# Kernel tuning notes

Measured on AMD Instinct MI355X. Metric: run time of the kernel, lower is better.

Reference implementation:

```python
import jax, jax.numpy as jnp
import numpy as np

N_NODES = 20000
N_EDGES = 320000
IN_DIM = 512
NUM_CLASSES = 10
DROP_P = 0.2


def _gcn_conv(x, src, dst, W, b, n):
    # PyG GCNConv: linear transform, add self-loops, symmetric deg^-1/2 norm,
    # scatter-add into destination nodes, then bias.
    h = x @ W                                   # [N, out]
    loops = jnp.arange(n)
    s = jnp.concatenate([src, loops])           # source (j)
    d = jnp.concatenate([dst, loops])           # destination (i)
    deg = jax.ops.segment_sum(jnp.ones_like(s, dtype=h.dtype), d, num_segments=n)
    dinv = jax.lax.rsqrt(deg)                   # deg >= 1 thanks to self-loops
    norm = dinv[s] * dinv[d]                    # [E+N]
    msg = h[s] * norm[:, None]                  # gather + per-edge scale
    out = jax.ops.segment_sum(msg, d, num_segments=n)  # scatter-add
    return out + b


def _dropout(x, key, p=DROP_P):
    keep = jax.random.bernoulli(key, 1.0 - p, x.shape)
    return jnp.where(keep, x / (1.0 - p), jnp.zeros((), x.dtype))


def setup_inputs() -> dict:
    key = jax.random.key(0)
    ks = jax.random.split(key, 6)
    x = jax.random.normal(ks[0], (N_NODES, IN_DIM), dtype=jnp.float32)
    edge_index = jax.random.randint(ks[1], (2, N_EDGES), 0, N_NODES, dtype=jnp.int64)
    h1, h2 = IN_DIM // 2, IN_DIM // 4
    W1 = jax.random.normal(ks[2], (IN_DIM, h1), dtype=jnp.float32) / np.sqrt(IN_DIM)
    W2 = jax.random.normal(ks[3], (h1, h2), dtype=jnp.float32) / np.sqrt(h1)
    W3 = jax.random.normal(ks[4], (h2, NUM_CLASSES), dtype=jnp.float32) / np.sqrt(h2)
    b1 = jnp.zeros((h1,), jnp.float32)
    b2 = jnp.zeros((h2,), jnp.float32)
    b3 = jnp.zeros((NUM_CLASSES,), jnp.float32)
    return {"x": x, "edge_index": edge_index, "W1": W1, "b1": b1,
            "W2": W2, "b2": b2, "W3": W3, "b3": b3}


def reference(x, edge_index, W1, b1, W2, b2, W3, b3):
    n = x.shape[0]
    src, dst = edge_index[0], edge_index[1]
    dk1, dk2 = jax.random.split(jax.random.key(1))
    h = _gcn_conv(x, src, dst, W1, b1, n)
    h = _dropout(jax.nn.relu(h), dk1)
    h = _gcn_conv(h, src, dst, W2, b2, n)
    h = _dropout(jax.nn.relu(h), dk2)
    h = _gcn_conv(h, src, dst, W3, b3, n)
    return jax.nn.log_softmax(h, axis=1)
```

## Files before the change

kernel.cpp:

```cpp
#include <hip/hip_runtime.h>
#include <hip/hip_bf16.h>
#include <math.h>

typedef __attribute__((ext_vector_type(8))) short short8;
typedef __attribute__((ext_vector_type(8))) unsigned short ushort8;
typedef __attribute__((ext_vector_type(4))) float f32x4;

__host__ __device__ inline void threefry2x32(unsigned k0, unsigned k1,
                                             unsigned x0, unsigned x1,
                                             unsigned* out0, unsigned* out1) {
  unsigned ks0 = k0, ks1 = k1, ks2 = k0 ^ k1 ^ 0x1BD11BDAu;
  x0 += ks0; x1 += ks1;
#define TF_ROUND(r) { x0 += x1; x1 = (x1 << (r)) | (x1 >> (32 - (r))); x1 ^= x0; }
  TF_ROUND(13) TF_ROUND(15) TF_ROUND(26) TF_ROUND(6)
  x0 += ks1; x1 += ks2 + 1u;
  TF_ROUND(17) TF_ROUND(29) TF_ROUND(16) TF_ROUND(24)
  x0 += ks2; x1 += ks0 + 2u;
  TF_ROUND(13) TF_ROUND(15) TF_ROUND(26) TF_ROUND(6)
  x0 += ks0; x1 += ks1 + 3u;
  TF_ROUND(17) TF_ROUND(29) TF_ROUND(16) TF_ROUND(24)
  x0 += ks1; x1 += ks2 + 4u;
  TF_ROUND(13) TF_ROUND(15) TF_ROUND(26) TF_ROUND(6)
  x0 += ks2; x1 += ks0 + 5u;
#undef TF_ROUND
  *out0 = x0; *out1 = x1;
}

__device__ inline float jax_uniform01(unsigned key0, unsigned key1, unsigned i) {
  unsigned o0, o1;
  threefry2x32(key0, key1, 0u, i, &o0, &o1);
  unsigned bits = o0 ^ o1;
  return __uint_as_float((bits >> 9) | 0x3f800000u) - 1.0f;
}

__device__ inline unsigned short f2bf(float f) {
  unsigned u = __float_as_uint(f);
  u += 0x7fffu + ((u >> 16) & 1u);
  return (unsigned short)(u >> 16);
}

__device__ inline float bf2f(unsigned short b) {
  return __uint_as_float(((unsigned)b) << 16);
}

__global__ __launch_bounds__(256) void k_init(int* __restrict__ deg, int n,
                                              const float* __restrict__ W1,
                                              unsigned short* __restrict__ W1T,
                                              const float* __restrict__ W2,
                                              unsigned short* __restrict__ W2T) {
  const int S1 = 512 * 256, S2 = 256 * 128;
  int idx = blockIdx.x * 256 + threadIdx.x;
  if (idx < n) { deg[idx] = 0; return; }
  idx -= n;
  if (idx < S1) {
    int k = idx / 256, c = idx % 256;
    W1T[(size_t)c * 512 + k] = f2bf(W1[idx]);
    return;
  }
  idx -= S1;
  if (idx < S2) {
    int k = idx / 128, c = idx % 128;
    W2T[(size_t)c * 256 + k] = f2bf(W2[idx]);
  }
}

__global__ void k_deg(const int* __restrict__ ei, int E, int* __restrict__ deg) {
  int e = blockIdx.x * blockDim.x + threadIdx.x;
  if (e >= E) return;
  atomicAdd(&deg[ei[E + e]], 1);
}

__global__ __launch_bounds__(256) void k_bsum(const int* __restrict__ deg,
                                              int* __restrict__ bsum, int n) {
  int i = blockIdx.x * 256 + threadIdx.x;
  int v = (i < n) ? deg[i] : 0;
#pragma unroll
  for (int o = 32; o; o >>= 1) v += __shfl_down(v, o);
  __shared__ int ws[4];
  if ((threadIdx.x & 63) == 0) ws[threadIdx.x >> 6] = v;
  __syncthreads();
  if (threadIdx.x == 0) bsum[blockIdx.x] = ws[0] + ws[1] + ws[2] + ws[3];
}

__global__ __launch_bounds__(256) void k_scatter2(const int* __restrict__ deg,
                                                  const int* __restrict__ bsum,
                                                  int* __restrict__ off, int* __restrict__ cur,
                                                  float* __restrict__ dinv, int n) {
  int i = blockIdx.x * 256 + threadIdx.x;
  int lane = threadIdx.x & 63, w = threadIdx.x >> 6;
  int pb = 0;
  for (int k = lane; k < blockIdx.x; k += 64) pb += bsum[k];
#pragma unroll
  for (int o = 32; o; o >>= 1) pb += __shfl_xor(pb, o);

  int d = (i < n) ? deg[i] : 0;
  int inc = d;
#pragma unroll
  for (int o = 1; o < 64; o <<= 1) {
    int u = __shfl_up(inc, o);
    if (lane >= o) inc += u;
  }
  __shared__ int wsum[4];
  if (lane == 63) wsum[w] = inc;
  __syncthreads();
  int wbase = 0;
  for (int k = 0; k < w; ++k) wbase += wsum[k];
  int excl = inc - d + wbase + pb;
  if (i < n) {
    off[i] = excl;
    cur[i] = excl;
    dinv[i] = 1.0f / sqrtf((float)(d + 1));
    if (i == n - 1) off[n] = excl + d;
  }
}

__global__ void k_fill_w(const int* __restrict__ ei, int E,
                         int* __restrict__ cur, int* __restrict__ srcs,
                         float* __restrict__ wgt, const float* __restrict__ dinv) {
  int e = blockIdx.x * blockDim.x + threadIdx.x;
  if (e >= E) return;
  int s = ei[e];
  int d = ei[E + e];
  int pos = atomicAdd(&cur[d], 1);
  srcs[pos] = s;
  wgt[pos] = dinv[s] * dinv[d];
}

template <int NF, bool AF32, bool OBF>
__global__ __launch_bounds__(256) void k_gemm_mfma(const void* __restrict__ Ap,
                                                   const unsigned short* __restrict__ BT,
                                                   void* __restrict__ Cp,
                                                   int M, int N, int K) {
  constexpr int BN = 32 * NF;
  __shared__ unsigned short As[64][40];
  __shared__ unsigned short Bs[BN][40];
  const int tid = threadIdx.x;
  const int row0 = blockIdx.y * 64;
  const int col0 = blockIdx.x * BN;
  const int w = tid >> 6, lane = tid & 63;
  const int wm = w >> 1, wn = w & 1;
  const int lr = lane & 15, lk = lane >> 4;

  f32x4 acc[2][NF];
#pragma unroll
  for (int mi = 0; mi < 2; ++mi)
#pragma unroll
    for (int ni = 0; ni < NF; ++ni) acc[mi][ni] = (f32x4)0.0f;

  const int ar = tid >> 2;
  const int aseg = (tid & 3) * 8;

  for (int k0 = 0; k0 < K; k0 += 32) {
    {
      int grow = row0 + ar;
      ushort8 av = (ushort8)0;
      if (grow < M) {
        if (AF32) {
          const float* A = (const float*)Ap;
          const float* p = &A[(size_t)grow * K + k0 + aseg];
          float4 v0 = *(const float4*)p;
          float4 v1 = *(const float4*)(p + 4);
          av[0] = f2bf(v0.x); av[1] = f2bf(v0.y); av[2] = f2bf(v0.z); av[3] = f2bf(v0.w);
          av[4] = f2bf(v1.x); av[5] = f2bf(v1.y); av[6] = f2bf(v1.z); av[7] = f2bf(v1.w);
        } else {
          const unsigned short* A = (const unsigned short*)Ap;
          av = *(const ushort8*)&A[(size_t)grow * K + k0 + aseg];
        }
      }
      *(ushort8*)&As[ar][aseg] = av;
    }
#pragma unroll
    for (int p = 0; p < BN / 64; ++p) {
      int u = tid + p * 256;
      int br = u >> 2;
      int bseg = (u & 3) * 8;
      ushort8 bv = *(const ushort8*)&BT[(size_t)(col0 + br) * K + k0 + bseg];
      *(ushort8*)&Bs[br][bseg] = bv;
    }
    __syncthreads();

    short8 a[2], b[NF];
#pragma unroll
    for (int mi = 0; mi < 2; ++mi)
      a[mi] = *(const short8*)&As[wm * 32 + mi * 16 + lr][lk * 8];
#pragma unroll
    for (int ni = 0; ni < NF; ++ni)
      b[ni] = *(const short8*)&Bs[wn * (BN / 2) + ni * 16 + lr][lk * 8];
#pragma unroll
    for (int mi = 0; mi < 2; ++mi)
#pragma unroll
      for (int ni = 0; ni < NF; ++ni)
        acc[mi][ni] = __builtin_amdgcn_mfma_f32_16x16x32_bf16(a[mi], b[ni], acc[mi][ni], 0, 0, 0);
    __syncthreads();
  }

#pragma unroll
  for (int mi = 0; mi < 2; ++mi) {
    int rbase = row0 + wm * 32 + mi * 16 + lk * 4;
#pragma unroll
    for (int j = 0; j < 4; ++j) {
      int row = rbase + j;
      if (row < M) {
#pragma unroll
        for (int ni = 0; ni < NF; ++ni) {
          int col = col0 + wn * (BN / 2) + ni * 16 + lr;
          if (OBF) {
            ((unsigned short*)Cp)[(size_t)row * N + col] = f2bf(acc[mi][ni][j]);
          } else {
            ((float*)Cp)[(size_t)row * N + col] = acc[mi][ni][j];
          }
        }
      }
    }
  }
}

__global__ __launch_bounds__(256) void k_gemm(const float* __restrict__ A,
                                              const float* __restrict__ B,
                                              float* __restrict__ C,
                                              int M, int N, int K) {
  __shared__ float As[64][17];
  __shared__ float Bs[16][64];
  const int tid = threadIdx.x;
  const int tx = tid & 15, ty = tid >> 4;
  const int row0 = blockIdx.y * 64, col0 = blockIdx.x * 64;
  const int am = tid >> 2;
  const int aq = (tid & 3) * 4;
  const int bk = tid >> 4;
  const int bg = (tid & 15) * 4;
  const bool nvec = ((N & 3) == 0);
  float acc[4][4] = {{0.f}};

  for (int k0 = 0; k0 < K; k0 += 16) {
    {
      int row = row0 + am;
      if (row < M) {
        const float4 v = *reinterpret_cast<const float4*>(&A[(size_t)row * K + k0 + aq]);
        As[am][aq + 0] = v.x; As[am][aq + 1] = v.y;
        As[am][aq + 2] = v.z; As[am][aq + 3] = v.w;
      } else {
        As[am][aq + 0] = 0.f; As[am][aq + 1] = 0.f;
        As[am][aq + 2] = 0.f; As[am][aq + 3] = 0.f;
      }
    }
    {
      int krow = k0 + bk;
      if (nvec && (col0 + bg + 4 <= N)) {
        const float4 v = *reinterpret_cast<const float4*>(&B[(size_t)krow * N + col0 + bg]);
        Bs[bk][bg + 0] = v.x; Bs[bk][bg + 1] = v.y;
        Bs[bk][bg + 2] = v.z; Bs[bk][bg + 3] = v.w;
      } else {
        for (int j = 0; j < 4; ++j) {
          int col = col0 + bg + j;
          Bs[bk][bg + j] = (col < N) ? B[(size_t)krow * N + col] : 0.f;
        }
      }
    }
    __syncthreads();
#pragma unroll
    for (int kk = 0; kk < 16; ++kk) {
      float a0 = As[ty * 4 + 0][kk];
      float a1 = As[ty * 4 + 1][kk];
      float a2 = As[ty * 4 + 2][kk];
      float a3 = As[ty * 4 + 3][kk];
      float4 bv = *reinterpret_cast<const float4*>(&Bs[kk][tx * 4]);
      acc[0][0] += a0 * bv.x; acc[0][1] += a0 * bv.y; acc[0][2] += a0 * bv.z; acc[0][3] += a0 * bv.w;
      acc[1][0] += a1 * bv.x; acc[1][1] += a1 * bv.y; acc[1][2] += a1 * bv.z; acc[1][3] += a1 * bv.w;
      acc[2][0] += a2 * bv.x; acc[2][1] += a2 * bv.y; acc[2][2] += a2 * bv.z; acc[2][3] += a2 * bv.w;
      acc[3][0] += a3 * bv.x; acc[3][1] += a3 * bv.y; acc[3][2] += a3 * bv.z; acc[3][3] += a3 * bv.w;
    }
    __syncthreads();
  }

  for (int i = 0; i < 4; ++i) {
    int row = row0 + ty * 4 + i;
    if (row >= M) continue;
    for (int j = 0; j < 4; ++j) {
      int col = col0 + tx * 4 + j;
      if (col < N) C[(size_t)row * N + col] = acc[i][j];
    }
  }
}

template <int C, bool OBF>
__global__ __launch_bounds__(256) void k_agg_bf(const unsigned short* __restrict__ h,
                                                void* __restrict__ outv,
                                                const int* __restrict__ off,
                                                const int* __restrict__ srcs,
                                                const float* __restrict__ wgt,
                                                const float* __restrict__ dinv,
                                                const float* __restrict__ bias,
                                                unsigned key0, unsigned key1, int n) {
  typedef __attribute__((ext_vector_type(C))) unsigned short ushortC;
  const int node = blockIdx.x * (blockDim.x >> 6) + (threadIdx.x >> 6);
  if (node >= n) return;
  const int lane = threadIdx.x & 63;
  const int F = 64 * C;
  const float dv = dinv[node];

  float acc[C];
  {
    ushortC r = *(const ushortC*)(h + (size_t)node * F + lane * C);
    float wv = dv * dv;
#pragma unroll
    for (int j = 0; j < C; ++j) acc[j] = bf2f(r[j]) * wv;
  }
  int e = off[node];
  const int e1 = off[node + 1];
  for (; e + 8 <= e1; e += 8) {
    int s[8];
    float wv[8];
    ushortC r[8];
#pragma unroll
    for (int q = 0; q < 8; ++q) s[q] = srcs[e + q];
#pragma unroll
    for (int q = 0; q < 8; ++q) wv[q] = wgt[e + q];
#pragma unroll
    for (int q = 0; q < 8; ++q) r[q] = *(const ushortC*)(h + (size_t)s[q] * F + lane * C);
#pragma unroll
    for (int q = 0; q < 8; ++q)
#pragma unroll
      for (int j = 0; j < C; ++j) acc[j] += bf2f(r[q][j]) * wv[q];
  }
  for (; e < e1; ++e) {
    int s = srcs[e];
    float wv = wgt[e];
    ushortC r = *(const ushortC*)(h + (size_t)s * F + lane * C);
#pragma unroll
    for (int j = 0; j < C; ++j) acc[j] += bf2f(r[j]) * wv;
  }
#pragma unroll
  for (int j = 0; j < C; ++j) {
    float v = acc[j] + bias[lane * C + j];
    v = fmaxf(v, 0.0f);
    unsigned i = (unsigned)(node * F + lane * C + j);
    float u = jax_uniform01(key0, key1, i);
    v = (u < 0.8f) ? (v * 1.25f) : 0.0f;
    acc[j] = v;
  }
  if (OBF) {
    unsigned short* op = (unsigned short*)outv + (size_t)node * F + lane * C;
#pragma unroll
    for (int j = 0; j < C; ++j) op[j] = f2bf(acc[j]);
  } else {
    float* op = (float*)outv + (size_t)node * F + lane * C;
#pragma unroll
    for (int j = 0; j < C; ++j) op[j] = acc[j];
  }
}

__global__ __launch_bounds__(256) void k_agg3_lsm_v2(const float* __restrict__ h,
                                                     float* __restrict__ out,
                                                     const int* __restrict__ off,
                                                     const int* __restrict__ srcs,
                                                     const float* __restrict__ wgt,
                                                     const float* __restrict__ dinv,
                                                     const float* __restrict__ b,
                                                     int n) {
  const int node = blockIdx.x * 4 + (threadIdx.x >> 6);
  if (node >= n) return;
  const int lane = threadIdx.x & 63;
  const bool act = (lane < 10);
  const float dv = dinv[node];

  float acc = 0.0f;
  if (act) acc = h[(size_t)node * 10 + lane] * dv * dv;
  int e = off[node];
  const int e1 = off[node + 1];
  for (; e + 4 <= e1; e += 4) {
    int s0 = srcs[e + 0], s1 = srcs[e + 1], s2 = srcs[e + 2], s3 = srcs[e + 3];
    float w0 = wgt[e + 0], w1 = wgt[e + 1], w2 = wgt[e + 2], w3 = wgt[e + 3];
    if (act) {
      acc += h[(size_t)s0 * 10 + lane] * w0 + h[(size_t)s1 * 10 + lane] * w1 +
             h[(size_t)s2 * 10 + lane] * w2 + h[(size_t)s3 * 10 + lane] * w3;
    }
  }
  for (; e < e1; ++e) {
    int s = srcs[e];
    float w = wgt[e];
    if (act) acc += h[(size_t)s * 10 + lane] * w;
  }
  float v = act ? (acc + b[lane]) : -1e30f;
  float m = v;
#pragma unroll
  for (int o = 32; o; o >>= 1) m = fmaxf(m, __shfl_xor(m, o));
  float p = act ? expf(v - m) : 0.0f;
  float ssum = p;
#pragma unroll
  for (int o = 32; o; o >>= 1) ssum += __shfl_xor(ssum, o);
  float lse = m + logf(ssum);
  if (act) out[(size_t)node * 10 + lane] = v - lse;
}

extern "C" void kernel_launch(void* const* d_in, const int* in_sizes, int n_in,
                              void* d_out, int out_size, void* d_ws, size_t ws_size,
                              hipStream_t stream) {
  const float* x  = (const float*)d_in[0];
  const int*   ei = (const int*)d_in[1];
  const float* W1 = (const float*)d_in[2];
  const float* b1 = (const float*)d_in[3];
  const float* W2 = (const float*)d_in[4];
  const float* b2 = (const float*)d_in[5];
  const float* W3 = (const float*)d_in[6];
  const float* b3 = (const float*)d_in[7];
  float* out = (float*)d_out;

  const int N = 20000;
  const int E = in_sizes[1] / 2;
  const int D1 = 256, D2 = 128;
  const int NB = (N + 255) / 256;

  char* ws = (char*)d_ws;
  auto carve = [&](size_t bytes) -> char* {
    char* p = ws;
    ws += (bytes + 255) & ~(size_t)255;
    return p;
  };
  int*   deg  = (int*)carve((size_t)N * 4);
  int*   off  = (int*)carve((size_t)(N + 1) * 4);
  int*   cur  = (int*)carve((size_t)N * 4);
  float* dinv = (float*)carve((size_t)N * 4);
  int*   bsum = (int*)carve((size_t)128 * 4);
  int*   srcs = (int*)carve((size_t)E * 4);
  float* wgt  = (float*)carve((size_t)E * 4);
  unsigned short* W1T = (unsigned short*)carve((size_t)D1 * 512 * 2);
  unsigned short* W2T = (unsigned short*)carve((size_t)D2 * D1 * 2);
  unsigned short* bufHb = (unsigned short*)carve((size_t)N * D1 * 2);
  unsigned short* bufA_bf = (unsigned short*)carve((size_t)N * D1 * 2);
  float* bufA2 = (float*)bufA_bf;
  float* bufH3 = (float*)carve((size_t)N * 10 * 4);

  unsigned dk1_0, dk1_1, dk2_0, dk2_1;
  threefry2x32(0u, 1u, 0u, 0u, &dk1_0, &dk1_1);
  threefry2x32(0u, 1u, 0u, 1u, &dk2_0, &dk2_1);

  const int INIT_ITEMS = N + 512 * 256 + 256 * 128;
  k_init<<<(INIT_ITEMS + 255) / 256, 256, 0, stream>>>(deg, N, W1, W1T, W2, W2T);
  k_deg<<<(E + 255) / 256, 256, 0, stream>>>(ei, E, deg);
  k_bsum<<<NB, 256, 0, stream>>>(deg, bsum, N);
  k_scatter2<<<NB, 256, 0, stream>>>(deg, bsum, off, cur, dinv, N);
  k_fill_w<<<(E + 255) / 256, 256, 0, stream>>>(ei, E, cur, srcs, wgt, dinv);

  k_gemm_mfma<4, true, true><<<dim3(D1 / 128, (N + 63) / 64), 256, 0, stream>>>(x, W1T, bufHb, N, D1, 512);
  k_agg_bf<4, true><<<(N + 3) / 4, 256, 0, stream>>>(bufHb, bufA_bf, off, srcs, wgt, dinv, b1, dk1_0, dk1_1, N);

  k_gemm_mfma<4, false, true><<<dim3(D2 / 128, (N + 63) / 64), 256, 0, stream>>>(bufA_bf, W2T, bufHb, N, D2, D1);
  k_agg_bf<2, false><<<(N + 3) / 4, 256, 0, stream>>>(bufHb, bufA2, off, srcs, wgt, dinv, b2, dk2_0, dk2_1, N);

  k_gemm<<<dim3(1, (N + 63) / 64), 256, 0, stream>>>(bufA2, W3, bufH3, N, 10, D2);
  k_agg3_lsm_v2<<<(N + 3) / 4, 256, 0, stream>>>(bufH3, out, off, srcs, wgt, dinv, b3, N);
}
```

Baseline: 160.2 us.

## Fuse layer-2 aggregation with layer-3 linear and retile MFMA GEMM

Layer-2 aggregation, bias, ReLU and dropout are fused with the 128x10 layer-3 matmul. Each wavefront reduces its node's 128 features against W3 with shuffle reductions and writes only the 10 outputs. This removes the fp32 intermediate buffer round trip and the separate scalar GEMM kernel. The MFMA GEMM is also retiled to 32-row blocks covering the full output width, so A is read once per row block, at the cost of less reuse per block and a grid that assumes N is divisible by 32.

```diff
diff --git a/kernel.cpp b/kernel.cpp
--- a/kernel.cpp
+++ b/kernel.cpp
@@ -4,6 +4,7 @@
 
 typedef __attribute__((ext_vector_type(8))) short short8;
 typedef __attribute__((ext_vector_type(8))) unsigned short ushort8;
+typedef __attribute__((ext_vector_type(4))) unsigned short ushort4v;
 typedef __attribute__((ext_vector_type(4))) float f32x4;
 
 __host__ __device__ inline void threefry2x32(unsigned k0, unsigned k1,
@@ -126,48 +127,46 @@
   wgt[pos] = dinv[s] * dinv[d];
 }
 
-template <int NF, bool AF32, bool OBF>
+template <int BN, bool AF32, bool OBF>
 __global__ __launch_bounds__(256) void k_gemm_mfma(const void* __restrict__ Ap,
                                                    const unsigned short* __restrict__ BT,
                                                    void* __restrict__ Cp,
                                                    int M, int N, int K) {
-  constexpr int BN = 32 * NF;
-  __shared__ unsigned short As[64][40];
+  constexpr int WCOLS = BN / 4;
+  constexpr int NFW = WCOLS / 16;
+  __shared__ unsigned short As[32][40];
   __shared__ unsigned short Bs[BN][40];
   const int tid = threadIdx.x;
-  const int row0 = blockIdx.y * 64;
+  const int row0 = blockIdx.y * 32;
   const int col0 = blockIdx.x * BN;
-  const int w = tid >> 6, lane = tid & 63;
-  const int wm = w >> 1, wn = w & 1;
+  const int wn = tid >> 6, lane = tid & 63;
   const int lr = lane & 15, lk = lane >> 4;
 
-  f32x4 acc[2][NF];
+  f32x4 acc[2][NFW];
 #pragma unroll
   for (int mi = 0; mi < 2; ++mi)
 #pragma unroll
-    for (int ni = 0; ni < NF; ++ni) acc[mi][ni] = (f32x4)0.0f;
-
-  const int ar = tid >> 2;
-  const int aseg = (tid & 3) * 8;
+    for (int ni = 0; ni < NFW; ++ni) acc[mi][ni] = (f32x4)0.0f;
+
+  const int ar = tid >> 3;
+  const int aseg = (tid & 7) * 4;
 
   for (int k0 = 0; k0 < K; k0 += 32) {
     {
       int grow = row0 + ar;
-      ushort8 av = (ushort8)0;
+      unsigned short a4[4] = {0, 0, 0, 0};
       if (grow < M) {
         if (AF32) {
           const float* A = (const float*)Ap;
-          const float* p = &A[(size_t)grow * K + k0 + aseg];
-          float4 v0 = *(const float4*)p;
-          float4 v1 = *(const float4*)(p + 4);
-          av[0] = f2bf(v0.x); av[1] = f2bf(v0.y); av[2] = f2bf(v0.z); av[3] = f2bf(v0.w);
-          av[4] = f2bf(v1.x); av[5] = f2bf(v1.y); av[6] = f2bf(v1.z); av[7] = f2bf(v1.w);
+          float4 v = *(const float4*)&A[(size_t)grow * K + k0 + aseg];
+          a4[0] = f2bf(v.x); a4[1] = f2bf(v.y); a4[2] = f2bf(v.z); a4[3] = f2bf(v.w);
         } else {
           const unsigned short* A = (const unsigned short*)Ap;
-          av = *(const ushort8*)&A[(size_t)grow * K + k0 + aseg];
+          ushort4v v = *(const ushort4v*)&A[(size_t)grow * K + k0 + aseg];
+          a4[0] = v[0]; a4[1] = v[1]; a4[2] = v[2]; a4[3] = v[3];
         }
       }
-      *(ushort8*)&As[ar][aseg] = av;
+      *(ushort4v*)&As[ar][aseg] = *(ushort4v*)a4;
     }
 #pragma unroll
     for (int p = 0; p < BN / 64; ++p) {
@@ -179,31 +178,31 @@
     }
     __syncthreads();
 
-    short8 a[2], b[NF];
+    short8 a[2], b[NFW];
 #pragma unroll
     for (int mi = 0; mi < 2; ++mi)
-      a[mi] = *(const short8*)&As[wm * 32 + mi * 16 + lr][lk * 8];
-#pragma unroll
-    for (int ni = 0; ni < NF; ++ni)
-      b[ni] = *(const short8*)&Bs[wn * (BN / 2) + ni * 16 + lr][lk * 8];
+      a[mi] = *(const short8*)&As[mi * 16 + lr][lk * 8];
+#pragma unroll
+    for (int ni = 0; ni < NFW; ++ni)
+      b[ni] = *(const short8*)&Bs[wn * WCOLS + ni * 16 + lr][lk * 8];
 #pragma unroll
     for (int mi = 0; mi < 2; ++mi)
 #pragma unroll
-      for (int ni = 0; ni < NF; ++ni)
+      for (int ni = 0; ni < NFW; ++ni)
         acc[mi][ni] = __builtin_amdgcn_mfma_f32_16x16x32_bf16(a[mi], b[ni], acc[mi][ni], 0, 0, 0);
     __syncthreads();
   }
 
 #pragma unroll
   for (int mi = 0; mi < 2; ++mi) {
-    int rbase = row0 + wm * 32 + mi * 16 + lk * 4;
+    int rbase = row0 + mi * 16 + lk * 4;
 #pragma unroll
     for (int j = 0; j < 4; ++j) {
       int row = rbase + j;
       if (row < M) {
 #pragma unroll
-        for (int ni = 0; ni < NF; ++ni) {
-          int col = col0 + wn * (BN / 2) + ni * 16 + lr;
+        for (int ni = 0; ni < NFW; ++ni) {
+          int col = col0 + wn * WCOLS + ni * 16 + lr;
           if (OBF) {
             ((unsigned short*)Cp)[(size_t)row * N + col] = f2bf(acc[mi][ni][j]);
           } else {
@@ -211,73 +210,6 @@
           }
         }
       }
-    }
-  }
-}
-
-__global__ __launch_bounds__(256) void k_gemm(const float* __restrict__ A,
-                                              const float* __restrict__ B,
-                                              float* __restrict__ C,
-                                              int M, int N, int K) {
-  __shared__ float As[64][17];
-  __shared__ float Bs[16][64];
-  const int tid = threadIdx.x;
-  const int tx = tid & 15, ty = tid >> 4;
-  const int row0 = blockIdx.y * 64, col0 = blockIdx.x * 64;
-  const int am = tid >> 2;
-  const int aq = (tid & 3) * 4;
-  const int bk = tid >> 4;
-  const int bg = (tid & 15) * 4;
-  const bool nvec = ((N & 3) == 0);
-  float acc[4][4] = {{0.f}};
-
-  for (int k0 = 0; k0 < K; k0 += 16) {
-    {
-      int row = row0 + am;
-      if (row < M) {
-        const float4 v = *reinterpret_cast<const float4*>(&A[(size_t)row * K + k0 + aq]);
-        As[am][aq + 0] = v.x; As[am][aq + 1] = v.y;
-        As[am][aq + 2] = v.z; As[am][aq + 3] = v.w;
-      } else {
-        As[am][aq + 0] = 0.f; As[am][aq + 1] = 0.f;
-        As[am][aq + 2] = 0.f; As[am][aq + 3] = 0.f;
-      }
-    }
-    {
-      int krow = k0 + bk;
-      if (nvec && (col0 + bg + 4 <= N)) {
-        const float4 v = *reinterpret_cast<const float4*>(&B[(size_t)krow * N + col0 + bg]);
-        Bs[bk][bg + 0] = v.x; Bs[bk][bg + 1] = v.y;
-        Bs[bk][bg + 2] = v.z; Bs[bk][bg + 3] = v.w;
-      } else {
-        for (int j = 0; j < 4; ++j) {
-          int col = col0 + bg + j;
-          Bs[bk][bg + j] = (col < N) ? B[(size_t)krow * N + col] : 0.f;
-        }
-      }
-    }
-    __syncthreads();
-#pragma unroll
-    for (int kk = 0; kk < 16; ++kk) {
-      float a0 = As[ty * 4 + 0][kk];
-      float a1 = As[ty * 4 + 1][kk];
-      float a2 = As[ty * 4 + 2][kk];
-      float a3 = As[ty * 4 + 3][kk];
-      float4 bv = *reinterpret_cast<const float4*>(&Bs[kk][tx * 4]);
-      acc[0][0] += a0 * bv.x; acc[0][1] += a0 * bv.y; acc[0][2] += a0 * bv.z; acc[0][3] += a0 * bv.w;
-      acc[1][0] += a1 * bv.x; acc[1][1] += a1 * bv.y; acc[1][2] += a1 * bv.z; acc[1][3] += a1 * bv.w;
-      acc[2][0] += a2 * bv.x; acc[2][1] += a2 * bv.y; acc[2][2] += a2 * bv.z; acc[2][3] += a2 * bv.w;
-      acc[3][0] += a3 * bv.x; acc[3][1] += a3 * bv.y; acc[3][2] += a3 * bv.z; acc[3][3] += a3 * bv.w;
-    }
-    __syncthreads();
-  }
-
-  for (int i = 0; i < 4; ++i) {
-    int row = row0 + ty * 4 + i;
-    if (row >= M) continue;
-    for (int j = 0; j < 4; ++j) {
-      int col = col0 + tx * 4 + j;
-      if (col < N) C[(size_t)row * N + col] = acc[i][j];
     }
   }
 }
@@ -347,6 +279,85 @@
 #pragma unroll
     for (int j = 0; j < C; ++j) op[j] = acc[j];
   }
+}
+
+__global__ __launch_bounds__(256) void k_agg2_g3(const unsigned short* __restrict__ h,
+                                                 float* __restrict__ h3,
+                                                 const int* __restrict__ off,
+                                                 const int* __restrict__ srcs,
+                                                 const float* __restrict__ wgt,
+                                                 const float* __restrict__ dinv,
+                                                 const float* __restrict__ b2,
+                                                 const float* __restrict__ W3,
+                                                 unsigned key0, unsigned key1, int n) {
+  const int node = blockIdx.x * 4 + (threadIdx.x >> 6);
+  if (node >= n) return;
+  const int lane = threadIdx.x & 63;
+
+  float w3a[10], w3b[10];
+  {
+    const float4* p = (const float4*)(W3 + lane * 20);
+    float4 v0 = p[0], v1 = p[1], v2 = p[2], v3 = p[3], v4 = p[4];
+    w3a[0] = v0.x; w3a[1] = v0.y; w3a[2] = v0.z; w3a[3] = v0.w;
+    w3a[4] = v1.x; w3a[5] = v1.y; w3a[6] = v1.z; w3a[7] = v1.w;
+    w3a[8] = v2.x; w3a[9] = v2.y;
+    w3b[0] = v2.z; w3b[1] = v2.w;
+    w3b[2] = v3.x; w3b[3] = v3.y; w3b[4] = v3.z; w3b[5] = v3.w;
+    w3b[6] = v4.x; w3b[7] = v4.y; w3b[8] = v4.z; w3b[9] = v4.w;
+  }
+
+  const float dv = dinv[node];
+  float acc0, acc1;
+  {
+    unsigned r = *(const unsigned*)(h + (size_t)node * 128 + lane * 2);
+    float wv = dv * dv;
+    acc0 = bf2f((unsigned short)(r & 0xffffu)) * wv;
+    acc1 = bf2f((unsigned short)(r >> 16)) * wv;
+  }
+  int e = off[node];
+  const int e1 = off[node + 1];
+  for (; e + 8 <= e1; e += 8) {
+    int s[8];
+    float wv[8];
+    unsigned r[8];
+#pragma unroll
+    for (int q = 0; q < 8; ++q) s[q] = srcs[e + q];
+#pragma unroll
+    for (int q = 0; q < 8; ++q) wv[q] = wgt[e + q];
+#pragma unroll
+    for (int q = 0; q < 8; ++q) r[q] = *(const unsigned*)(h + (size_t)s[q] * 128 + lane * 2);
+#pragma unroll
+    for (int q = 0; q < 8; ++q) {
+      acc0 += bf2f((unsigned short)(r[q] & 0xffffu)) * wv[q];
+      acc1 += bf2f((unsigned short)(r[q] >> 16)) * wv[q];
+    }
+  }
+  for (; e < e1; ++e) {
+    int s = srcs[e];
+    float wv = wgt[e];
+    unsigned r = *(const unsigned*)(h + (size_t)s * 128 + lane * 2);
+    acc0 += bf2f((unsigned short)(r & 0xffffu)) * wv;
+    acc1 += bf2f((unsigned short)(r >> 16)) * wv;
+  }
+  {
+    float v = fmaxf(acc0 + b2[lane * 2], 0.0f);
+    float u = jax_uniform01(key0, key1, (unsigned)(node * 128 + lane * 2));
+    acc0 = (u < 0.8f) ? (v * 1.25f) : 0.0f;
+  }
+  {
+    float v = fmaxf(acc1 + b2[lane * 2 + 1], 0.0f);
+    float u = jax_uniform01(key0, key1, (unsigned)(node * 128 + lane * 2 + 1));
+    acc1 = (u < 0.8f) ? (v * 1.25f) : 0.0f;
+  }
+  float myout = 0.0f;
+#pragma unroll
+  for (int c = 0; c < 10; ++c) {
+    float part = acc0 * w3a[c] + acc1 * w3b[c];
+#pragma unroll
+    for (int o = 32; o; o >>= 1) part += __shfl_xor(part, o);
+    if (lane == c) myout = part;
+  }
+  if (lane < 10) h3[(size_t)node * 10 + lane] = myout;
 }
 
 __global__ __launch_bounds__(256) void k_agg3_lsm_v2(const float* __restrict__ h,
@@ -427,7 +438,6 @@
   unsigned short* W2T = (unsigned short*)carve((size_t)D2 * D1 * 2);
   unsigned short* bufHb = (unsigned short*)carve((size_t)N * D1 * 2);
   unsigned short* bufA_bf = (unsigned short*)carve((size_t)N * D1 * 2);
-  float* bufA2 = (float*)bufA_bf;
   float* bufH3 = (float*)carve((size_t)N * 10 * 4);
 
   unsigned dk1_0, dk1_1, dk2_0, dk2_1;
@@ -441,12 +451,11 @@
   k_scatter2<<<NB, 256, 0, stream>>>(deg, bsum, off, cur, dinv, N);
   k_fill_w<<<(E + 255) / 256, 256, 0, stream>>>(ei, E, cur, srcs, wgt, dinv);
 
-  k_gemm_mfma<4, true, true><<<dim3(D1 / 128, (N + 63) / 64), 256, 0, stream>>>(x, W1T, bufHb, N, D1, 512);
+  k_gemm_mfma<256, true, true><<<dim3(1, N / 32), 256, 0, stream>>>(x, W1T, bufHb, N, D1, 512);
   k_agg_bf<4, true><<<(N + 3) / 4, 256, 0, stream>>>(bufHb, bufA_bf, off, srcs, wgt, dinv, b1, dk1_0, dk1_1, N);
 
-  k_gemm_mfma<4, false, true><<<dim3(D2 / 128, (N + 63) / 64), 256, 0, stream>>>(bufA_bf, W2T, bufHb, N, D2, D1);
-  k_agg_bf<2, false><<<(N + 3) / 4, 256, 0, stream>>>(bufHb, bufA2, off, srcs, wgt, dinv, b2, dk2_0, dk2_1, N);
-
-  k_gemm<<<dim3(1, (N + 63) / 64), 256, 0, stream>>>(bufA2, W3, bufH3, N, 10, D2);
+  k_gemm_mfma<128, false, true><<<dim3(1, N / 32), 256, 0, stream>>>(bufA_bf, W2T, bufHb, N, D2, D1);
+  k_agg2_g3<<<(N + 3) / 4, 256, 0, stream>>>(bufHb, bufH3, off, srcs, wgt, dinv, b2, W3, dk2_0, dk2_1, N);
+
   k_agg3_lsm_v2<<<(N + 3) / 4, 256, 0, stream>>>(bufH3, out, off, srcs, wgt, dinv, b3, N);
 }
```

Result: faster. 151.9 us, median of 2 (-5.2%).
